# Kernel tuning notes

Hardware: AMD Instinct MI355X
Metric: run time of the kernel (lower is better)

Reference implementation:

```python
import jax, jax.numpy as jnp
import numpy as np

S = 512      # seq_length (fixed by generate_mask(m=512, n=512))
B = 16       # batch
H = 1024     # hidden_size
N = 16       # num_attention_heads
HD = H // N  # hidden per head = 64
DENSITY = 0.1  # sparsity = 0.9


def setup_inputs() -> dict:
    key = jax.random.key(0)
    k0, k1, k2, k3 = jax.random.split(key, 4)
    hidden_states = jax.random.normal(k0, (S, B, H), dtype=jnp.float32)
    attention_mask = jax.random.uniform(k1, (S, S)) < DENSITY
    attention_mask = attention_mask | jnp.eye(S, dtype=bool)  # no empty rows
    scale = 1.0 / np.sqrt(H).astype(np.float32)
    Wqkv = jax.random.normal(k2, (H, 3 * H), dtype=jnp.float32) * scale
    bqkv = jnp.zeros((3 * H,), dtype=jnp.float32)
    Wout = jax.random.normal(k3, (H, H), dtype=jnp.float32) * scale
    bout = jnp.zeros((H,), dtype=jnp.float32)
    return {"hidden_states": hidden_states, "attention_mask": attention_mask,
            "Wqkv": Wqkv, "bqkv": bqkv, "Wout": Wout, "bout": bout}


def reference(hidden_states, attention_mask, Wqkv, bqkv, Wout, bout):
    # hidden_states: [s, b, h] -> [b, s, h]
    x = jnp.transpose(hidden_states, (1, 0, 2))
    b = x.shape[0]
    # fused QKV projection, then per-head split of the last dim into (q,k,v) chunks
    qkv = (x @ Wqkv + bqkv).reshape(b, S, N, 3 * HD)
    q, k, v = qkv[..., :HD], qkv[..., HD:2 * HD], qkv[..., 2 * HD:]  # [b, s, n, hd]
    # SDDMM: scores only meaningful on mask nonzeros (dense-masked equivalent)
    scores = jnp.einsum('bind,bjnd->bnij', q, k) / np.sqrt(HD).astype(np.float32)
    neg = jnp.finfo(scores.dtype).min
    scores = jnp.where(attention_mask, scores, neg)
    # CSR softmax: softmax over the nonzeros of each row
    weights = jax.nn.softmax(scores, axis=-1)
    weights = jnp.where(attention_mask, weights, jnp.zeros((), scores.dtype))
    # SpMM: sparse weights @ dense values
    ctx = jnp.einsum('bnij,bjnd->bind', weights, v)  # [b, s, n, hd]
    # [b, s, n, hd] -> [s, b, n*hd]
    context = jnp.transpose(ctx, (1, 0, 2, 3)).reshape(S, b, H)
    return context @ Wout + bout  # [s, b, h]
```

## Files before the change

kernel.cpp:

```cpp
#include <hip/hip_runtime.h>
#include <hip/hip_bf16.h>

typedef __hip_bfloat16 bf16;
typedef unsigned short u16;
typedef unsigned int u32;
typedef unsigned long long u64;
typedef float f32x4 __attribute__((ext_vector_type(4)));
typedef short s16x8 __attribute__((ext_vector_type(8)));
typedef unsigned short u16x4 __attribute__((ext_vector_type(4)));

static constexpr int SQ    = 512;
static constexpr int BB    = 16;
static constexpr int HH    = 1024;
static constexpr int NHEAD = 16;
static constexpr int ROWS  = SQ * BB;
static constexpr int QKVC  = 3 * HH;

static constexpr long long OFF_FLAGS = 0;
static constexpr long long OFF_M16   = 4096;
static constexpr long long OFF_WQT   = 1048576;
static constexpr long long OFF_WOT   = OFF_WQT + (long long)QKVC * HH * 2;
static constexpr long long OFF_QK    = OFF_WOT + (long long)HH * HH * 2;
static constexpr long long OFF_VT    = OFF_QK + (long long)ROWS * 2048 * 2;
static constexpr long long OFF_CTX   = OFF_VT + (long long)256 * 64 * 512 * 2;

__device__ __forceinline__ float load_f(const void* p, long long i, int is_bf16) {
  if (is_bf16) return __bfloat162float(((const bf16*)p)[i]);
  return ((const float*)p)[i];
}
__device__ __forceinline__ u16 f2b(float x) { bf16 h = __float2bfloat16(x); return *(u16*)&h; }
__device__ __forceinline__ f32x4 mfma_bf16(s16x8 a, s16x8 b, f32x4 c) {
  return __builtin_amdgcn_mfma_f32_16x16x32_bf16(a, b, c, 0, 0, 0);
}
__device__ __forceinline__ void gll16(const void* g, void* lds) {
  __builtin_amdgcn_global_load_lds((const __attribute__((address_space(1))) unsigned int*)g,
                                   (__attribute__((address_space(3))) unsigned int*)lds, 16, 0, 0);
}
__device__ __forceinline__ u32 cvtpk(float lo, float hi) {
  u32 r;
  asm volatile("v_cvt_pk_bf16_f32 %0, %1, %2" : "=v"(r) : "v"(lo), "v"(hi));
  return r;
}
__device__ __forceinline__ void xcd_swz(int& bx, int& by) {
  int gx = gridDim.x;
  int nw = gx * gridDim.y;
  int lin = by * gx + bx;
  int q = nw >> 3;
  int nl = (lin & 7) * q + (lin >> 3);
  bx = nl % gx;
  by = nl / gx;
}
__device__ __forceinline__ int fl_from(const int* cnt) { return cnt[0] > 1800 ? 1 : 0; }
__device__ __forceinline__ int mm_from(const int* cnt) {
  if (cnt[1] == 0)      return (cnt[4] > 0) ? 0 : 1;
  if (cnt[2] >= cnt[3]) return 2;
  if (cnt[5] == 0)      return 3;
  return 4;
}

__global__ __launch_bounds__(256) void sa_detect_part(const void* hs, const void* mask, int* cnt) {
  __shared__ int lc[6];
  if (threadIdx.x < 6) lc[threadIdx.x] = 0;
  __syncthreads();
  int gid = blockIdx.x * 256 + threadIdx.x;
  if (gid < 2048) {
    unsigned short v = ((const unsigned short*)hs)[2 * gid];
    float f = __uint_as_float(((unsigned)v) << 16);
    float a = fabsf(f);
    if (v == 0 || (a > 1e-9f && a < 1e4f)) atomicAdd(&lc[0], 1);
  }
  const unsigned char* mb = (const unsigned char*)mask;
  int codd = 0, c1 = 0, c3f = 0, c48 = 0, cb1 = 0;
  #pragma unroll
  for (int r = 0; r < 4; ++r) {
    int i = gid * 4 + r;
    int base = i * 4;
    unsigned char b1 = mb[base + 1], b3 = mb[base + 3];
    if (b1 | b3) codd++;
    if (b1) cb1++;
    if (b1 == 1) c1++;
    if (b3 == 1) c1++;
    if (b1 == 0x3f) c3f++;
    if (b3 == 0x3f) c3f++;
    if (i & 1) { if (mb[base]) c48++; }
  }
  atomicAdd(&lc[1], codd);
  atomicAdd(&lc[2], c1);
  atomicAdd(&lc[3], c3f);
  atomicAdd(&lc[4], c48);
  atomicAdd(&lc[5], cb1);
  __syncthreads();
  if (threadIdx.x < 6) atomicAdd(&cnt[threadIdx.x], lc[threadIdx.x]);
}

__global__ __launch_bounds__(256) void sa_maskexp(const void* mask, u16* m16, const int* cnt) {
  int idx = blockIdx.x * 256 + threadIdx.x;
  int i = idx >> 9, c = idx & 511;
  int jw = c >> 5, r = c & 31;
  int g = r >> 3, q = r & 7;
  int t = q >> 2, rr = q & 3;
  long long j = (long long)i * 512 + jw * 32 + t * 16 + 4 * g + rr;
  int mm = mm_from(cnt);
  bool v;
  if      (mm == 0) v = ((const int*)mask)[j] != 0;
  else if (mm == 1) v = ((const long long*)mask)[j] != 0;
  else if (mm == 2) v = ((const unsigned char*)mask)[j] != 0;
  else if (mm == 3) v = ((const float*)mask)[j] != 0.0f;
  else              v = ((const unsigned short*)mask)[j] != 0;
  m16[idx] = v ? 0xFFFFu : 0u;
}

__global__ __launch_bounds__(256) void sa_cvt_hs(const void* hs, u16* hsb, const int* cnt) {
  if (fl_from(cnt)) return;
  int tid = blockIdx.x * 256 + threadIdx.x;
  int row = tid >> 7, u7 = tid & 127;
  int sc = u7 >> 3, u = u7 & 7;
  long long ebase = (long long)row * 1024 + sc * 64 + u * 8;
  const float4* pf = (const float4*)((const float*)hs + ebase);
  float4 x0 = pf[0], x1 = pf[1];
  s16x8 ov;
  ov[0] = f2b(x0.x); ov[1] = f2b(x0.y); ov[2] = f2b(x0.z); ov[3] = f2b(x0.w);
  ov[4] = f2b(x1.x); ov[5] = f2b(x1.y); ov[6] = f2b(x1.z); ov[7] = f2b(x1.w);
  *(s16x8*)((char*)hsb + (long long)row * 2048 + sc * 128 + ((u ^ (row & 7)) * 16)) = ov;
}

__global__ __launch_bounds__(256) void sa_wtransc2(const void* Wq, u16* WqT, const void* Wo, u16* WoT,
                                                   const int* cnt) {
  const void* W; u16* WT; int Nld;
  if (blockIdx.z == 0) { W = Wq; WT = WqT; Nld = QKVC; }
  else                 { if (blockIdx.x >= HH / 256) return; W = Wo; WT = WoT; Nld = HH; }
  int nrow = blockIdx.x * 256 + threadIdx.x;
  int sc = blockIdx.y >> 3, u = blockIdx.y & 7;
  int kb = sc * 64 + u * 8;
  const int fl = fl_from(cnt);
  s16x8 ov;
  #pragma unroll
  for (int e = 0; e < 8; ++e) ov[e] = f2b(load_f(W, (long long)(kb + e) * Nld + nrow, fl));
  *(s16x8*)((char*)WT + (long long)nrow * 2048 + sc * 128 + ((u ^ (nrow & 7)) * 16)) = ov;
}

__global__ __launch_bounds__(256) void mm_qkv(const u16* __restrict__ hs, const u16* __restrict__ hsb,
                                              const u16* __restrict__ BT, const void* bias,
                                              u16* qk, u16* V, const int* cnt) {
  __shared__ u16 As[128 * 64];
  __shared__ u16 Bs[128 * 64];
  const int tid = threadIdx.x, w = tid >> 6, lane = tid & 63;
  const int g = lane >> 4, li = lane & 15;
  int bx = blockIdx.x, by = blockIdx.y;
  xcd_swz(bx, by);
  const int m0 = by * 128, n0 = bx * 128;
  const int wm = (w >> 1) * 64, wn = (w & 1) * 64;
  const int K = 1024;
  const int fl = fl_from(cnt);
  f32x4 acc[4][4] = {};
  for (int k0 = 0; k0 < K; k0 += 64) {
    if (k0) __syncthreads();
    #pragma unroll
    for (int q = 0; q < 4; ++q) {
      int c = w * 4 + q;
      int r = c * 8 + (lane >> 3);
      const u16* asrc = fl ? (hs  + (long long)(m0 + r) * K + k0 + (((lane & 7) ^ (r & 7)) * 8))
                           : (hsb + (long long)(m0 + r) * K + k0 + ((lane & 7) * 8));
      gll16(asrc, &As[c * 512]);
      gll16(BT + (long long)(n0 + r) * K + k0 + (lane & 7) * 8, &Bs[c * 512]);
    }
    __syncthreads();
    #pragma unroll
    for (int ks = 0; ks < 2; ++ks) {
      s16x8 af[4], bfr[4];
      #pragma unroll
      for (int mi = 0; mi < 4; ++mi) {
        int r = wm + mi * 16 + li;
        int off = (ks * 64 + g * 16) ^ ((r & 7) << 4);
        af[mi] = *(const s16x8*)((const char*)As + r * 128 + off);
      }
      #pragma unroll
      for (int nj = 0; nj < 4; ++nj) {
        int r = wn + nj * 16 + li;
        int off = (ks * 64 + g * 16) ^ ((r & 7) << 4);
        bfr[nj] = *(const s16x8*)((const char*)Bs + r * 128 + off);
      }
      #pragma unroll
      for (int mi = 0; mi < 4; ++mi)
        #pragma unroll
        for (int nj = 0; nj < 4; ++nj)
          acc[mi][nj] = mfma_bf16(af[mi], bfr[nj], acc[mi][nj]);
    }
  }
  const int s0 = (m0 + wm) >> 4;
  #pragma unroll
  for (int nj = 0; nj < 4; ++nj) {
    int colbase = n0 + wn + nj * 16;
    int col = colbase + li;
    float bv = load_f(bias, col, fl);
    int c16 = colbase >> 4;
    int ht = c16 % 12, n = c16 / 12;
    int colmod = (ht * 16) + li;
    if (ht < 8) {
      #pragma unroll
      for (int mi = 0; mi < 4; ++mi) {
        int s = s0 + mi;
        #pragma unroll
        for (int rr = 0; rr < 4; ++rr) {
          int b = 4 * g + rr;
          qk[((long long)(b * 512 + s)) * 2048 + n * 128 + colmod] =
              f2b(acc[mi][nj][rr] + bv);
        }
      }
    } else {
      int d = colmod - 128;
      #pragma unroll
      for (int rr = 0; rr < 4; ++rr) {
        int b = 4 * g + rr;
        #pragma unroll
        for (int mi = 0; mi < 4; ++mi)
          V[((long long)(b * 16 + n)) * 32768 + (s0 + mi) * 64 + d] =
              f2b(acc[mi][nj][rr] + bv);
      }
    }
  }
}

__global__ __launch_bounds__(1024) void sa_attn7(const u16* __restrict__ qk, const u16* __restrict__ V,
                                                 const u16* __restrict__ m16, u16* __restrict__ ctx) {
  __shared__ __align__(16) u16 SHM[81920];
  u16* const Ks = SHM;
  u16* const Vs = SHM + 32768;
  u16* const PB = SHM + 65536;

  const int tid = threadIdx.x, w = tid >> 6, lane = tid & 63;
  const int g = lane >> 4, li = lane & 15;
  const int n = blockIdx.x, b = blockIdx.y;

  const u16* kg = qk + (long long)(b * 512) * 2048 + n * 128 + 64;
  #pragma unroll
  for (int it = 0; it < 4; ++it) {
    int lin = it * 1024 + tid;
    int s = lin >> 3, c = lin & 7;
    s16x8 kv = *(const s16x8*)(kg + (long long)s * 2048 + c * 8);
    *(s16x8*)(Ks + s * 64 + ((c ^ (s & 7)) * 8)) = kv;
  }
  const u16* vg = V + (long long)(b * 16 + n) * 32768;
  #pragma unroll
  for (int q = 0; q < 4; ++q) {
    int lin = q * 1024 + tid;
    int s = lin >> 3, dc = lin & 7;
    s16x8 v = *(const s16x8*)(vg + s * 64 + dc * 8);
    #pragma unroll
    for (int e = 0; e < 8; ++e) {
      int d = dc * 8 + e;
      Vs[d * 512 + (((s >> 3) ^ e ^ dc) * 8) + (s & 7)] = v[e];
    }
  }
  __syncthreads();

  const int i0 = w * 32;
  s16x8 qf0[2], qf1[2];
  #pragma unroll
  for (int tl = 0; tl < 2; ++tl) {
    const u16* qb = qk + ((long long)(b * 512 + i0 + tl * 16 + li)) * 2048 + n * 128;
    qf0[tl] = *(const s16x8*)(qb + g * 8);
    qf1[tl] = *(const s16x8*)(qb + 32 + g * 8);
  }
  s16x8 af1;
  #pragma unroll
  for (int e = 0; e < 8; ++e) af1[e] = (li == 0) ? (short)0x3F80 : (short)0;

  char* const pw = (char*)PB + w * 2048;
  const float SC  = 0.125f * 1.44269504f;
  const float THR = 44.3614f;

  const u16* mk0 = m16 + (long long)(i0 + li) * 512 + g * 8;
  const u16* mk1 = m16 + (long long)(i0 + 16 + li) * 512 + g * 8;

  f32x4 cacc[2][4] = {};
  f32x4 lacc[2] = {};
  float m[2] = {-1e30f, -1e30f};

  for (int jw = 0; jw < 16; ++jw) {
    uint4 mmv[2];
    mmv[0] = *(const uint4*)(mk0 + jw * 32);
    mmv[1] = *(const uint4*)(mk1 + jw * 32);
    s16x8 kf0[2], kf1[2];
    #pragma unroll
    for (int t = 0; t < 2; ++t) {
      int j = jw * 32 + t * 16 + li;
      const u16* kb = Ks + j * 64;
      kf0[t] = *(const s16x8*)(kb + ((g ^ (j & 7)) * 8));
      kf1[t] = *(const s16x8*)(kb + (((4 + g) ^ (j & 7)) * 8));
    }
    f32x4 sa[2][2];
    #pragma unroll
    for (int tl = 0; tl < 2; ++tl)
      #pragma unroll
      for (int t = 0; t < 2; ++t) {
        f32x4 z = {};
        z = mfma_bf16(kf0[t], qf0[tl], z);
        z = mfma_bf16(kf1[t], qf1[tl], z);
        sa[tl][t] = z;
      }
    s16x8 pf[2];
    #pragma unroll
    for (int tl = 0; tl < 2; ++tl) {
      float pm = fmaxf(fmaxf(fmaxf(sa[tl][0][0], sa[tl][0][1]), fmaxf(sa[tl][0][2], sa[tl][0][3])),
                       fmaxf(fmaxf(sa[tl][1][0], sa[tl][1][1]), fmaxf(sa[tl][1][2], sa[tl][1][3])));
      pm = fmaxf(pm, __shfl_xor(pm, 16));
      pm = fmaxf(pm, __shfl_xor(pm, 32));
      if (__any(pm > m[tl] + THR)) {
        float mn = fmaxf(m[tl], pm);
        float sc = __builtin_exp2f((m[tl] - mn) * SC);
        lacc[tl] *= sc;
        #pragma unroll
        for (int dt = 0; dt < 4; ++dt) cacc[tl][dt] *= sc;
        m[tl] = mn;
      }
      float mv = m[tl];
      float p0 = __builtin_exp2f((sa[tl][0][0] - mv) * SC);
      float p1 = __builtin_exp2f((sa[tl][0][1] - mv) * SC);
      float p2 = __builtin_exp2f((sa[tl][0][2] - mv) * SC);
      float p3 = __builtin_exp2f((sa[tl][0][3] - mv) * SC);
      float p4 = __builtin_exp2f((sa[tl][1][0] - mv) * SC);
      float p5 = __builtin_exp2f((sa[tl][1][1] - mv) * SC);
      float p6 = __builtin_exp2f((sa[tl][1][2] - mv) * SC);
      float p7 = __builtin_exp2f((sa[tl][1][3] - mv) * SC);
      u32 r0 = cvtpk(p0, p1) & mmv[tl].x;
      u32 r1 = cvtpk(p2, p3) & mmv[tl].y;
      u32 r2 = cvtpk(p4, p5) & mmv[tl].z;
      u32 r3 = cvtpk(p6, p7) & mmv[tl].w;
      char* pt = pw + tl * 1024 + li * 64;
      *(uint2*)(pt + ((g ^ (li & 6)) * 8))       = make_uint2(r0, r1);
      *(uint2*)(pt + (((4 + g) ^ (li & 6)) * 8)) = make_uint2(r2, r3);
      pf[tl] = *(const s16x8*)(pw + tl * 1024 + li * 64 + (((2 * g) ^ (li & 6)) * 8));
      lacc[tl] = mfma_bf16(af1, pf[tl], lacc[tl]);
    }
    #pragma unroll
    for (int dt = 0; dt < 4; ++dt) {
      int d = dt * 16 + li;
      s16x8 vf = *(const s16x8*)(Vs + d * 512 +
                                 (((jw * 4 + g) ^ (d & 7) ^ ((d >> 3) & 7)) * 8));
      #pragma unroll
      for (int tl = 0; tl < 2; ++tl)
        cacc[tl][dt] = mfma_bf16(vf, pf[tl], cacc[tl][dt]);
    }
  }
  #pragma unroll
  for (int tl = 0; tl < 2; ++tl) {
    float lv = __shfl(lacc[tl][0], li);
    float inv = 1.0f / lv;
    #pragma unroll
    for (int dt = 0; dt < 4; ++dt) {
      u32 lo = cvtpk(cacc[tl][dt][0] * inv, cacc[tl][dt][1] * inv);
      u32 hi = cvtpk(cacc[tl][dt][2] * inv, cacc[tl][dt][3] * inv);
      *(uint2*)(pw + li * 128 + (((dt * 4 + g) ^ ((li & 7) << 1)) * 8)) = make_uint2(lo, hi);
    }
    int il = lane >> 2;
    #pragma unroll
    for (int p = 0; p < 2; ++p) {
      int c = (lane & 3) + p * 4;
      s16x8 v = *(const s16x8*)(pw + il * 128 + (((2 * c) ^ ((il & 7) << 1)) * 8));
      *(s16x8*)(ctx + ((long long)((i0 + tl * 16 + il) * 16 + b)) * 1024 + n * 64 +
                ((c ^ (b & 7)) * 8)) = v;
    }
  }
}

__global__ __launch_bounds__(256) void mm_out(const u16* __restrict__ Asrc, const u16* __restrict__ BT,
                                              const void* bias, void* out, const int* cnt) {
  __shared__ u16 As[128 * 64];
  __shared__ u16 Bs[128 * 64];
  const int tid = threadIdx.x, w = tid >> 6, lane = tid & 63;
  const int g = lane >> 4, li = lane & 15;
  int bx = blockIdx.x, by = blockIdx.y;
  xcd_swz(bx, by);
  const int m0 = by * 128, n0 = bx * 128;
  const int wm = (w >> 1) * 64, wn = (w & 1) * 64;
  const int K = 1024;
  f32x4 acc[4][4] = {};
  for (int k0 = 0; k0 < K; k0 += 64) {
    if (k0) __syncthreads();
    #pragma unroll
    for (int q = 0; q < 4; ++q) {
      int c = w * 4 + q;
      int r = c * 8 + (lane >> 3);
      gll16(Asrc + (long long)(m0 + r) * K + k0 + (lane & 7) * 8, &As[c * 512]);
      gll16(BT   + (long long)(n0 + r) * K + k0 + (lane & 7) * 8, &Bs[c * 512]);
    }
    __syncthreads();
    #pragma unroll
    for (int ks = 0; ks < 2; ++ks) {
      s16x8 af[4], bfr[4];
      #pragma unroll
      for (int mi = 0; mi < 4; ++mi) {
        int r = wm + mi * 16 + li;
        int off = (ks * 64 + g * 16) ^ ((r & 7) << 4);
        af[mi] = *(const s16x8*)((const char*)As + r * 128 + off);
      }
      #pragma unroll
      for (int nj = 0; nj < 4; ++nj) {
        int r = wn + nj * 16 + li;
        int off = (ks * 64 + g * 16) ^ ((r & 7) << 4);
        bfr[nj] = *(const s16x8*)((const char*)Bs + r * 128 + off);
      }
      #pragma unroll
      for (int mi = 0; mi < 4; ++mi)
        #pragma unroll
        for (int nj = 0; nj < 4; ++nj)
          acc[mi][nj] = mfma_bf16(af[mi], bfr[nj], acc[mi][nj]);
    }
  }
  const int fl = fl_from(cnt);
  #pragma unroll
  for (int nj = 0; nj < 4; ++nj) {
    int col = n0 + wn + nj * 16 + li;
    float bv = load_f(bias, col, fl);
    #pragma unroll
    for (int mi = 0; mi < 4; ++mi) {
      #pragma unroll
      for (int rr = 0; rr < 4; ++rr) {
        long long row = m0 + wm + mi * 16 + 4 * g + rr;
        float v = acc[mi][nj][rr] + bv;
        if (fl) ((u16*)out)[row * 1024 + col] = f2b(v);
        else    ((float*)out)[row * 1024 + col] = v;
      }
    }
  }
}

extern "C" void kernel_launch(void* const* d_in, const int* in_sizes, int n_in,
                              void* d_out, int out_size, void* d_ws, size_t ws_size,
                              hipStream_t stream) {
  const void* hs   = d_in[0];
  const void* mask = d_in[1];
  const void* Wqkv = d_in[2];
  const void* bqkv = d_in[3];
  const void* Wout = d_in[4];
  const void* bout = d_in[5];

  char* ws = (char*)d_ws;
  int* cnt   = (int*)(ws + 64);
  u16* m16   = (u16*)(ws + OFF_M16);
  u16* WqkvT = (u16*)(ws + OFF_WQT);
  u16* WoutT = (u16*)(ws + OFF_WOT);
  u16* qk    = (u16*)(ws + OFF_QK);
  u16* V     = (u16*)(ws + OFF_VT);
  u16* ctx   = (u16*)(ws + OFF_CTX);
  u16* hsb   = ctx;

  hipMemsetAsync(cnt, 0, 64, stream);
  sa_detect_part<<<64, 256, 0, stream>>>(hs, mask, cnt);
  sa_maskexp<<<1024, 256, 0, stream>>>(mask, m16, cnt);
  sa_cvt_hs<<<(ROWS * 128) / 256, 256, 0, stream>>>(hs, hsb, cnt);
  sa_wtransc2<<<dim3(QKVC / 256, 128, 2), 256, 0, stream>>>(Wqkv, WqkvT, Wout, WoutT, cnt);

  mm_qkv<<<dim3(QKVC / 128, ROWS / 128), 256, 0, stream>>>(
      (const u16*)hs, hsb, WqkvT, bqkv, qk, V, cnt);
  sa_attn7<<<dim3(NHEAD, BB), 1024, 0, stream>>>(qk, V, m16, ctx);
  mm_out<<<dim3(HH / 128, ROWS / 128), 256, 0, stream>>>(ctx, WoutT, bout, d_out, cnt);
}
```

Before: 177.5 us.

## Double-buffer LDS in the QKV and output GEMMs and merge preprocessing kernels

Both bf16 MFMA GEMMs now use two LDS buffers. The next K-slice's global-to-LDS loads are issued before computing on the current slice, with one barrier per iteration instead of two. This aims to overlap memory latency with MFMA work, but doubles LDS per block to 64KB, which may lower occupancy. Separately, the mask expansion, weight transpose/convert and hidden-state conversion kernels are merged into one launch, with the hidden-state part doing 8 chunks per block, to cut launch overhead.

Result: no change. 175.2 us (-1.3%).

```diff
diff --git a/kernel.cpp b/kernel.cpp
--- a/kernel.cpp
+++ b/kernel.cpp
@@ -16,7 +16,6 @@
 static constexpr int ROWS  = SQ * BB;
 static constexpr int QKVC  = 3 * HH;
 
-static constexpr long long OFF_FLAGS = 0;
 static constexpr long long OFF_M16   = 4096;
 static constexpr long long OFF_WQT   = 1048576;
 static constexpr long long OFF_WOT   = OFF_WQT + (long long)QKVC * HH * 2;
@@ -93,57 +92,64 @@
   if (threadIdx.x < 6) atomicAdd(&cnt[threadIdx.x], lc[threadIdx.x]);
 }
 
-__global__ __launch_bounds__(256) void sa_maskexp(const void* mask, u16* m16, const int* cnt) {
-  int idx = blockIdx.x * 256 + threadIdx.x;
-  int i = idx >> 9, c = idx & 511;
-  int jw = c >> 5, r = c & 31;
-  int g = r >> 3, q = r & 7;
-  int t = q >> 2, rr = q & 3;
-  long long j = (long long)i * 512 + jw * 32 + t * 16 + 4 * g + rr;
-  int mm = mm_from(cnt);
-  bool v;
-  if      (mm == 0) v = ((const int*)mask)[j] != 0;
-  else if (mm == 1) v = ((const long long*)mask)[j] != 0;
-  else if (mm == 2) v = ((const unsigned char*)mask)[j] != 0;
-  else if (mm == 3) v = ((const float*)mask)[j] != 0.0f;
-  else              v = ((const unsigned short*)mask)[j] != 0;
-  m16[idx] = v ? 0xFFFFu : 0u;
-}
-
-__global__ __launch_bounds__(256) void sa_cvt_hs(const void* hs, u16* hsb, const int* cnt) {
+__global__ __launch_bounds__(256) void sa_preproc(const void* mask, u16* m16,
+                                                  const void* Wq, u16* WqT,
+                                                  const void* Wo, u16* WoT,
+                                                  const void* hs, u16* hsb, const int* cnt) {
+  int blk = blockIdx.x;
+  if (blk < 1024) {
+    int idx = blk * 256 + threadIdx.x;
+    int i = idx >> 9, c = idx & 511;
+    int jw = c >> 5, r = c & 31;
+    int g = r >> 3, q = r & 7;
+    int t = q >> 2, rr = q & 3;
+    long long j = (long long)i * 512 + jw * 32 + t * 16 + 4 * g + rr;
+    int mm = mm_from(cnt);
+    bool v;
+    if      (mm == 0) v = ((const int*)mask)[j] != 0;
+    else if (mm == 1) v = ((const long long*)mask)[j] != 0;
+    else if (mm == 2) v = ((const unsigned char*)mask)[j] != 0;
+    else if (mm == 3) v = ((const float*)mask)[j] != 0.0f;
+    else              v = ((const unsigned short*)mask)[j] != 0;
+    m16[idx] = v ? 0xFFFFu : 0u;
+    return;
+  }
+  if (blk < 1024 + 1536 + 512) {
+    const void* W; u16* WT; int Nld; int idx;
+    if (blk < 1024 + 1536) { idx = blk - 1024;        W = Wq; WT = WqT; Nld = QKVC; }
+    else                   { idx = blk - 1024 - 1536; W = Wo; WT = WoT; Nld = HH; }
+    int xb = idx % (Nld / 256), yb = idx / (Nld / 256);
+    int nrow = xb * 256 + threadIdx.x;
+    int sc = yb >> 3, u = yb & 7;
+    int kb = sc * 64 + u * 8;
+    const int fl = fl_from(cnt);
+    s16x8 ov;
+    #pragma unroll
+    for (int e = 0; e < 8; ++e) ov[e] = f2b(load_f(W, (long long)(kb + e) * Nld + nrow, fl));
+    *(s16x8*)((char*)WT + (long long)nrow * 2048 + sc * 128 + ((u ^ (nrow & 7)) * 16)) = ov;
+    return;
+  }
   if (fl_from(cnt)) return;
-  int tid = blockIdx.x * 256 + threadIdx.x;
-  int row = tid >> 7, u7 = tid & 127;
-  int sc = u7 >> 3, u = u7 & 7;
-  long long ebase = (long long)row * 1024 + sc * 64 + u * 8;
-  const float4* pf = (const float4*)((const float*)hs + ebase);
-  float4 x0 = pf[0], x1 = pf[1];
-  s16x8 ov;
-  ov[0] = f2b(x0.x); ov[1] = f2b(x0.y); ov[2] = f2b(x0.z); ov[3] = f2b(x0.w);
-  ov[4] = f2b(x1.x); ov[5] = f2b(x1.y); ov[6] = f2b(x1.z); ov[7] = f2b(x1.w);
-  *(s16x8*)((char*)hsb + (long long)row * 2048 + sc * 128 + ((u ^ (row & 7)) * 16)) = ov;
-}
-
-__global__ __launch_bounds__(256) void sa_wtransc2(const void* Wq, u16* WqT, const void* Wo, u16* WoT,
-                                                   const int* cnt) {
-  const void* W; u16* WT; int Nld;
-  if (blockIdx.z == 0) { W = Wq; WT = WqT; Nld = QKVC; }
-  else                 { if (blockIdx.x >= HH / 256) return; W = Wo; WT = WoT; Nld = HH; }
-  int nrow = blockIdx.x * 256 + threadIdx.x;
-  int sc = blockIdx.y >> 3, u = blockIdx.y & 7;
-  int kb = sc * 64 + u * 8;
-  const int fl = fl_from(cnt);
-  s16x8 ov;
-  #pragma unroll
-  for (int e = 0; e < 8; ++e) ov[e] = f2b(load_f(W, (long long)(kb + e) * Nld + nrow, fl));
-  *(s16x8*)((char*)WT + (long long)nrow * 2048 + sc * 128 + ((u ^ (nrow & 7)) * 16)) = ov;
+  int base = blk - (1024 + 1536 + 512);
+  for (int it = 0; it < 8; ++it) {
+    int tid = (base * 8 + it) * 256 + threadIdx.x;
+    int row = tid >> 7, u7 = tid & 127;
+    int sc = u7 >> 3, u = u7 & 7;
+    long long ebase = (long long)row * 1024 + sc * 64 + u * 8;
+    const float4* pf = (const float4*)((const float*)hs + ebase);
+    float4 x0 = pf[0], x1 = pf[1];
+    s16x8 ov;
+    ov[0] = f2b(x0.x); ov[1] = f2b(x0.y); ov[2] = f2b(x0.z); ov[3] = f2b(x0.w);
+    ov[4] = f2b(x1.x); ov[5] = f2b(x1.y); ov[6] = f2b(x1.z); ov[7] = f2b(x1.w);
+    *(s16x8*)((char*)hsb + (long long)row * 2048 + sc * 128 + ((u ^ (row & 7)) * 16)) = ov;
+  }
 }
 
 __global__ __launch_bounds__(256) void mm_qkv(const u16* __restrict__ hs, const u16* __restrict__ hsb,
                                               const u16* __restrict__ BT, const void* bias,
                                               u16* qk, u16* V, const int* cnt) {
-  __shared__ u16 As[128 * 64];
-  __shared__ u16 Bs[128 * 64];
+  __shared__ u16 As[2][128 * 64];
+  __shared__ u16 Bs[2][128 * 64];
   const int tid = threadIdx.x, w = tid >> 6, lane = tid & 63;
   const int g = lane >> 4, li = lane & 15;
   int bx = blockIdx.x, by = blockIdx.y;
@@ -152,19 +158,29 @@
   const int wm = (w >> 1) * 64, wn = (w & 1) * 64;
   const int K = 1024;
   const int fl = fl_from(cnt);
-  f32x4 acc[4][4] = {};
-  for (int k0 = 0; k0 < K; k0 += 64) {
-    if (k0) __syncthreads();
+
+  const int c_ = w * 4;
+  const int r0_ = (lane >> 3);
+  auto STAGE = [&](int buf, int k0) {
     #pragma unroll
     for (int q = 0; q < 4; ++q) {
-      int c = w * 4 + q;
-      int r = c * 8 + (lane >> 3);
+      int c = c_ + q;
+      int r = c * 8 + r0_;
       const u16* asrc = fl ? (hs  + (long long)(m0 + r) * K + k0 + (((lane & 7) ^ (r & 7)) * 8))
                            : (hsb + (long long)(m0 + r) * K + k0 + ((lane & 7) * 8));
-      gll16(asrc, &As[c * 512]);
-      gll16(BT + (long long)(n0 + r) * K + k0 + (lane & 7) * 8, &Bs[c * 512]);
-    }
-    __syncthreads();
+      gll16(asrc, &As[buf][c * 512]);
+      gll16(BT + (long long)(n0 + r) * K + k0 + (lane & 7) * 8, &Bs[buf][c * 512]);
+    }
+  };
+
+  f32x4 acc[4][4] = {};
+  STAGE(0, 0);
+  __syncthreads();
+  int cur = 0;
+  for (int k0 = 0; k0 < K; k0 += 64) {
+    if (k0 + 64 < K) STAGE(cur ^ 1, k0 + 64);
+    const u16* Ab = As[cur];
+    const u16* Bb = Bs[cur];
     #pragma unroll
     for (int ks = 0; ks < 2; ++ks) {
       s16x8 af[4], bfr[4];
@@ -172,13 +188,13 @@
       for (int mi = 0; mi < 4; ++mi) {
         int r = wm + mi * 16 + li;
         int off = (ks * 64 + g * 16) ^ ((r & 7) << 4);
-        af[mi] = *(const s16x8*)((const char*)As + r * 128 + off);
+        af[mi] = *(const s16x8*)((const char*)Ab + r * 128 + off);
       }
       #pragma unroll
       for (int nj = 0; nj < 4; ++nj) {
         int r = wn + nj * 16 + li;
         int off = (ks * 64 + g * 16) ^ ((r & 7) << 4);
-        bfr[nj] = *(const s16x8*)((const char*)Bs + r * 128 + off);
+        bfr[nj] = *(const s16x8*)((const char*)Bb + r * 128 + off);
       }
       #pragma unroll
       for (int mi = 0; mi < 4; ++mi)
@@ -186,6 +202,8 @@
         for (int nj = 0; nj < 4; ++nj)
           acc[mi][nj] = mfma_bf16(af[mi], bfr[nj], acc[mi][nj]);
     }
+    __syncthreads();
+    cur ^= 1;
   }
   const int s0 = (m0 + wm) >> 4;
   #pragma unroll
@@ -366,8 +384,8 @@
 
 __global__ __launch_bounds__(256) void mm_out(const u16* __restrict__ Asrc, const u16* __restrict__ BT,
                                               const void* bias, void* out, const int* cnt) {
-  __shared__ u16 As[128 * 64];
-  __shared__ u16 Bs[128 * 64];
+  __shared__ u16 As[2][128 * 64];
+  __shared__ u16 Bs[2][128 * 64];
   const int tid = threadIdx.x, w = tid >> 6, lane = tid & 63;
   const int g = lane >> 4, li = lane & 15;
   int bx = blockIdx.x, by = blockIdx.y;
@@ -375,17 +393,25 @@
   const int m0 = by * 128, n0 = bx * 128;
   const int wm = (w >> 1) * 64, wn = (w & 1) * 64;
   const int K = 1024;
+  const int c_ = w * 4;
+  const int r0_ = (lane >> 3);
+  auto STAGE = [&](int buf, int k0) {
+    #pragma unroll
+    for (int q = 0; q < 4; ++q) {
+      int c = c_ + q;
+      int r = c * 8 + r0_;
+      gll16(Asrc + (long long)(m0 + r) * K + k0 + (lane & 7) * 8, &As[buf][c * 512]);
+      gll16(BT   + (long long)(n0 + r) * K + k0 + (lane & 7) * 8, &Bs[buf][c * 512]);
+    }
+  };
   f32x4 acc[4][4] = {};
+  STAGE(0, 0);
+  __syncthreads();
+  int cur = 0;
   for (int k0 = 0; k0 < K; k0 += 64) {
-    if (k0) __syncthreads();
-    #pragma unroll
-    for (int q = 0; q < 4; ++q) {
-      int c = w * 4 + q;
-      int r = c * 8 + (lane >> 3);
-      gll16(Asrc + (long long)(m0 + r) * K + k0 + (lane & 7) * 8, &As[c * 512]);
-      gll16(BT   + (long long)(n0 + r) * K + k0 + (lane & 7) * 8, &Bs[c * 512]);
-    }
-    __syncthreads();
+    if (k0 + 64 < K) STAGE(cur ^ 1, k0 + 64);
+    const u16* Ab = As[cur];
+    const u16* Bb = Bs[cur];
     #pragma unroll
     for (int ks = 0; ks < 2; ++ks) {
       s16x8 af[4], bfr[4];
@@ -393,13 +419,13 @@
       for (int mi = 0; mi < 4; ++mi) {
         int r = wm + mi * 16 + li;
         int off = (ks * 64 + g * 16) ^ ((r & 7) << 4);
-        af[mi] = *(const s16x8*)((const char*)As + r * 128 + off);
+        af[mi] = *(const s16x8*)((const char*)Ab + r * 128 + off);
       }
       #pragma unroll
       for (int nj = 0; nj < 4; ++nj) {
         int r = wn + nj * 16 + li;
         int off = (ks * 64 + g * 16) ^ ((r & 7) << 4);
-        bfr[nj] = *(const s16x8*)((const char*)Bs + r * 128 + off);
+        bfr[nj] = *(const s16x8*)((const char*)Bb + r * 128 + off);
       }
       #pragma unroll
       for (int mi = 0; mi < 4; ++mi)
@@ -407,6 +433,8 @@
         for (int nj = 0; nj < 4; ++nj)
           acc[mi][nj] = mfma_bf16(af[mi], bfr[nj], acc[mi][nj]);
     }
+    __syncthreads();
+    cur ^= 1;
   }
   const int fl = fl_from(cnt);
   #pragma unroll
@@ -448,9 +476,7 @@
 
   hipMemsetAsync(cnt, 0, 64, stream);
   sa_detect_part<<<64, 256, 0, stream>>>(hs, mask, cnt);
-  sa_maskexp<<<1024, 256, 0, stream>>>(mask, m16, cnt);
-  sa_cvt_hs<<<(ROWS * 128) / 256, 256, 0, stream>>>(hs, hsb, cnt);
-  sa_wtransc2<<<dim3(QKVC / 256, 128, 2), 256, 0, stream>>>(Wqkv, WqkvT, Wout, WoutT, cnt);
+  sa_preproc<<<3584, 256, 0, stream>>>(mask, m16, Wqkv, WqkvT, Wout, WoutT, hs, hsb, cnt);
 
   mm_qkv<<<dim3(QKVC / 128, ROWS / 128), 256, 0, stream>>>(
       (const u16*)hs, hsb, WqkvT, bqkv, qk, V, cnt);
```
